# Kernel tuning notes

Measured on AMD Instinct MI355X. Metric: run time of the kernel, lower is better.

The kernel has to match this reference:

```python
import jax, jax.numpy as jnp
import numpy as np

B = 8
M = 500_000
XSIZE = 128


def setup_inputs() -> dict:
    key = jax.random.key(0)
    k1, k2 = jax.random.split(key)
    indices = jax.random.randint(k1, (B, M, 3), 0, XSIZE, dtype=jnp.int32)
    values = jax.random.normal(k2, (B, M), dtype=jnp.float32)
    return {"indices": indices, "values": values, "xsize": XSIZE}


def reference(indices, values, xsize):
    # Batched scatter-add density accumulation (tensor_scatter_nd_add per sample)
    def scatter_one(idx, val):
        grid = jnp.zeros((xsize, xsize, xsize), dtype=val.dtype)
        return grid.at[idx[:, 0], idx[:, 1], idx[:, 2]].add(val)

    grid = jax.vmap(scatter_one)(indices, values)  # (B, X, X, X)

    # Adjacent voxel differences along each spatial axis
    d1 = grid[:, 1:, :, :] - grid[:, :-1, :, :]
    d2 = grid[:, :, 1:, :] - grid[:, :, :-1, :]
    d3 = grid[:, :, :, 1:] - grid[:, :, :, :-1]

    ax = (1, 2, 3)
    # Total variation loss: normalized by total voxel count xsize^3
    num_pixels = jnp.float32(xsize * xsize * xsize)
    tv = (jnp.sum(jnp.abs(d1), axis=ax)
          + jnp.sum(jnp.abs(d2), axis=ax)
          + jnp.sum(jnp.abs(d3), axis=ax)) / num_pixels

    # MSE smoothness loss: normalizer matches TF code (2*X*X - X - X)
    num_pairs = jnp.float32(2 * xsize * xsize - 2 * xsize)
    mse = (jnp.sum(jnp.square(d1), axis=ax)
           + jnp.sum(jnp.square(d2), axis=ax)
           + jnp.sum(jnp.square(d3), axis=ax)) / num_pairs

    return jnp.stack([tv, mse])  # (2, B)
```

## Files before the change

### kernel.cpp

```cpp
#include <hip/hip_runtime.h>
#include <stdint.h>

#define BATCH 8
#define MPTS 500000
#define NPTS (BATCH * MPTS)
#define NBQ 1024
#define TP 16384
#define NTILE ((NPTS + TP - 1) / TP)
#define HROW (NBQ + 1)
#define NIFACE 304
#define NBND (BATCH * NIFACE)

template <int NT>
__device__ __forceinline__ void block_reduce2(float& tv, float& mse) {
    for (int off = 32; off > 0; off >>= 1) {
        tv  += __shfl_down(tv, off, 64);
        mse += __shfl_down(mse, off, 64);
    }
    __shared__ float stv[NT / 64], sms[NT / 64];
    int w = threadIdx.x >> 6, lane = threadIdx.x & 63;
    if (lane == 0) { stv[w] = tv; sms[w] = mse; }
    __syncthreads();
    if (threadIdx.x == 0) {
        float a = 0.f, m = 0.f;
        #pragma unroll
        for (int e = 0; e < NT / 64; ++e) { a += stv[e]; m += sms[e]; }
        tv = a; mse = m;
    }
}

__device__ __forceinline__ uint32_t pack_aux(int b, int i, int j, int k) {
    uint32_t q = ((uint32_t)b << 7) | ((uint32_t)(i >> 5) << 5) |
                 ((uint32_t)(j >> 5) << 3) | (uint32_t)(k >> 4);
    uint32_t l = ((uint32_t)(i & 31) << 9) | ((uint32_t)(j & 31) << 4) | (uint32_t)(k & 15);
    return (q << 14) | l;
}

__device__ __forceinline__ int gaddr(int s, int kl) {
    return s * 16 + (kl & 3) + ((((kl >> 2) ^ (s >> 1)) & 3) << 2);
}
__device__ __forceinline__ int goff(int s, int c) {
    return ((c ^ (s >> 1)) & 3) << 2;
}

__device__ __forceinline__ uint32_t val16(float f) {
    return (__float_as_uint(f) + 0x8000u) >> 16;
}

__global__ void __launch_bounds__(1024, 8) sort_k(const int* __restrict__ idx,
                                                  const float* __restrict__ val,
                                                  uint32_t* __restrict__ hoff,
                                                  uint32_t* __restrict__ rec) {
    __shared__ uint32_t h[NBQ];
    __shared__ uint32_t wtot[16];
    __shared__ uint32_t srt[TP];
    int tile = blockIdx.x;
    int p0 = tile * TP;
    int cnt = min(TP, NPTS - p0);
    h[threadIdx.x] = 0;
    __syncthreads();
    uint32_t a[16]; uint32_t vpk[8];
    int ng = cnt >> 2;
    #pragma unroll
    for (int e = 0; e < 4; ++e) {
        int g = threadIdx.x + e * 1024;
        if (g < ng) {
            int p = p0 + g * 4;
            const int4* ip = (const int4*)(idx + (size_t)p * 3);
            int4 A = ip[0], B = ip[1], C = ip[2];
            float4 V = *(const float4*)(val + p);
            int b = p / MPTS;
            a[4*e+0] = pack_aux(b, A.x, A.y, A.z);
            a[4*e+1] = pack_aux(b, A.w, B.x, B.y);
            a[4*e+2] = pack_aux(b, B.z, B.w, C.x);
            a[4*e+3] = pack_aux(b, C.y, C.z, C.w);
            vpk[2*e]     = val16(V.x) | (val16(V.y) << 16);
            vpk[2*e + 1] = val16(V.z) | (val16(V.w) << 16);
            #pragma unroll
            for (int u = 0; u < 4; ++u) atomicAdd(&h[a[4*e+u] >> 14], 1u);
        } else {
            a[4*e+0] = a[4*e+1] = a[4*e+2] = a[4*e+3] = 0xFFFFFFFFu;
            vpk[2*e] = vpk[2*e + 1] = 0u;
        }
    }
    __syncthreads();
    int q = threadIdx.x, lane = q & 63, wave = q >> 6;
    uint32_t cq = h[q];
    uint32_t inc = cq;
    #pragma unroll
    for (int off = 1; off < 64; off <<= 1) {
        uint32_t n = __shfl_up(inc, off, 64);
        if (lane >= off) inc += n;
    }
    if (lane == 63) wtot[wave] = inc;
    __syncthreads();
    if (q < 16) {
        uint32_t w = wtot[q];
        #pragma unroll
        for (int off = 1; off < 16; off <<= 1) {
            uint32_t n = __shfl_up(w, off, 16);
            if (q >= off) w += n;
        }
        wtot[q] = w;
    }
    __syncthreads();
    uint32_t lstart = (wave ? wtot[wave - 1] : 0u) + inc - cq;
    hoff[(size_t)tile * HROW + q] = lstart;
    if (q == 0) hoff[(size_t)tile * HROW + NBQ] = (uint32_t)cnt;
    h[q] = lstart;
    __syncthreads();
    #pragma unroll
    for (int e = 0; e < 16; ++e) {
        if (a[e] != 0xFFFFFFFFu) {
            uint32_t qq = a[e] >> 14;
            uint32_t u = (vpk[e >> 1] >> ((e & 1) * 16)) & 0xFFFFu;
            srt[atomicAdd(&h[qq], 1u)] = (u << 16) | (a[e] & 16383u);
        }
    }
    __syncthreads();
    uint4* recq = (uint4*)(rec + (size_t)tile * TP);
    const uint4* sr4 = (const uint4*)srt;
    for (int s = threadIdx.x; s < (cnt >> 2); s += 1024) recq[s] = sr4[s];
}

__global__ void __launch_bounds__(1024, 8) accum_k(const uint32_t* __restrict__ rec,
                                                   const uint32_t* __restrict__ hoff,
                                                   uint16_t* __restrict__ faces,
                                                   float2* __restrict__ pa) {
    __shared__ float g[16384];
    int qb = blockIdx.x;
    {
        float4 z = make_float4(0.f, 0.f, 0.f, 0.f);
        #pragma unroll
        for (int c = 0; c < 4; ++c)
            *(float4*)&g[(threadIdx.x + c * 1024) * 4] = z;
    }
    __syncthreads();
    {
        int grp = threadIdx.x >> 3;
        int r8  = threadIdx.x & 7;
        const uint32_t* rowA = hoff + (size_t)grp * HROW;
        uint32_t a0 = rowA[qb], a1 = rowA[qb + 1];
        const uint32_t* rpA = rec + (size_t)grp * TP;
        int tB = grp + 128;
        uint32_t b0 = 0, b1 = 0;
        const uint32_t* rpB = nullptr;
        if (tB < NTILE) {
            const uint32_t* rowB = hoff + (size_t)tB * HROW;
            b0 = rowB[qb]; b1 = rowB[qb + 1];
            rpB = rec + (size_t)tB * TP;
        }
        for (uint32_t r = a0 + r8; r < a1; r += 8) {
            uint32_t e = rpA[r];
            int l = e & 16383;
            atomicAdd(&g[gaddr(l >> 4, l & 15)], __uint_as_float(e & 0xFFFF0000u));
        }
        if (rpB) {
            for (uint32_t r = b0 + r8; r < b1; r += 8) {
                uint32_t e = rpB[r];
                int l = e & 16383;
                atomicAdd(&g[gaddr(l >> 4, l & 15)], __uint_as_float(e & 0xFFFF0000u));
            }
        }
    }
    __syncthreads();
    float tv = 0.f, mse = 0.f;
    {
        int s = threadIdx.x;
        int jl = s & 31, il = s >> 5;
        bool jin = jl < 31, iin = il < 31;
        float own[16];
        #pragma unroll
        for (int c = 0; c < 4; ++c)
            *(float4*)&own[c * 4] = *(const float4*)&g[s * 16 + goff(s, c)];
        #pragma unroll
        for (int k = 0; k < 15; ++k) {
            float d = own[k + 1] - own[k]; tv += fabsf(d); mse += d * d;
        }
        #pragma unroll
        for (int hh = 0; hh < 2; ++hh) {
            if (jin) {
                float jn[8];
                *(float4*)&jn[0] = *(const float4*)&g[(s + 1) * 16 + goff(s + 1, 2 * hh)];
                *(float4*)&jn[4] = *(const float4*)&g[(s + 1) * 16 + goff(s + 1, 2 * hh + 1)];
                #pragma unroll
                for (int k = 0; k < 8; ++k) {
                    float d = jn[k] - own[8 * hh + k]; tv += fabsf(d); mse += d * d;
                }
            }
            if (iin) {
                float inb[8];
                *(float4*)&inb[0] = *(const float4*)&g[(s + 32) * 16 + goff(s + 32, 2 * hh)];
                *(float4*)&inb[4] = *(const float4*)&g[(s + 32) * 16 + goff(s + 32, 2 * hh + 1)];
                #pragma unroll
                for (int k = 0; k < 8; ++k) {
                    float d = inb[k] - own[8 * hh + k]; tv += fabsf(d); mse += d * d;
                }
            }
        }
    }
    {
        uint16_t* f = faces + (size_t)qb * 4096;
        int t = threadIdx.x;
        if (t < 512) {
            int hi = t >> 4, lo = t & 15;
            f[t]        = (uint16_t)(__float_as_uint(g[gaddr(hi, lo)]) >> 16);
            f[512 + t]  = (uint16_t)(__float_as_uint(g[gaddr(992 + hi, lo)]) >> 16);
            f[1024 + t] = (uint16_t)(__float_as_uint(g[gaddr(hi * 32, lo)]) >> 16);
            f[1536 + t] = (uint16_t)(__float_as_uint(g[gaddr(hi * 32 + 31, lo)]) >> 16);
        }
        f[2048 + t] = (uint16_t)(__float_as_uint(g[gaddr(t, 0)]) >> 16);
        f[3072 + t] = (uint16_t)(__float_as_uint(g[gaddr(t, 15)]) >> 16);
    }
    block_reduce2<1024>(tv, mse);
    if (threadIdx.x == 0) pa[qb] = make_float2(tv, mse);
}

__device__ __forceinline__ float f16up(uint16_t u) {
    return __uint_as_float(((uint32_t)u) << 16);
}

__global__ void __launch_bounds__(256) boundary_k(const uint16_t* __restrict__ faces,
                                                  float2* __restrict__ pb) {
    int x = blockIdx.x;
    int b = x / NIFACE;
    int r = x - b * NIFACE;
    int qA, qB, fA, fB, elems;
    if (r < 96) {
        int s = r >> 5, u = (r >> 3) & 3, w = r & 7;
        qA = (b << 7) | (s << 5) | (u << 3) | w; qB = qA + 32;
        fA = 512; fB = 0; elems = 512;
    } else if (r < 192) {
        int r2 = r - 96;
        int s = r2 >> 5, u = (r2 >> 3) & 3, w = r2 & 7;
        qA = (b << 7) | (u << 5) | (s << 3) | w; qB = qA + 8;
        fA = 1536; fB = 1024; elems = 512;
    } else {
        int r2 = r - 192;
        int s = r2 >> 4, u = (r2 >> 2) & 3, v = r2 & 3;
        qA = (b << 7) | (u << 5) | (v << 3) | s; qB = qA + 1;
        fA = 3072; fB = 2048; elems = 1024;
    }
    const uint16_t* pA = faces + (size_t)qA * 4096 + fA;
    const uint16_t* pB = faces + (size_t)qB * 4096 + fB;
    float tv = 0.f, mse = 0.f;
    for (int e = threadIdx.x; e < elems; e += 256) {
        float d = f16up(pB[e]) - f16up(pA[e]);
        tv += fabsf(d); mse += d * d;
    }
    block_reduce2<256>(tv, mse);
    if (threadIdx.x == 0) pb[x] = make_float2(tv, mse);
}

__global__ void __launch_bounds__(256) final_k(const float2* __restrict__ pa,
                                               const float2* __restrict__ pb,
                                               float* __restrict__ out) {
    int b = blockIdx.x;
    float tv = 0.f, mse = 0.f;
    const float2* a = pa + (size_t)b * (NBQ / BATCH);
    for (int i = threadIdx.x; i < NBQ / BATCH; i += 256) { float2 v = a[i]; tv += v.x; mse += v.y; }
    const float2* p = pb + (size_t)b * NIFACE;
    for (int i = threadIdx.x; i < NIFACE; i += 256) { float2 v = p[i]; tv += v.x; mse += v.y; }
    block_reduce2<256>(tv, mse);
    if (threadIdx.x == 0) {
        out[b]     = tv  * (1.f / 2097152.f);
        out[8 + b] = mse * (1.f / 32512.f);
    }
}

extern "C" void kernel_launch(void* const* d_in, const int* in_sizes, int n_in,
                              void* d_out, int out_size, void* d_ws, size_t ws_size,
                              hipStream_t stream) {
    const int*   indices = (const int*)d_in[0];
    const float* values  = (const float*)d_in[1];
    float*       out     = (float*)d_out;

    char* wp = (char*)d_ws;
    uint32_t* hoff  = (uint32_t*)wp;
    wp += (((size_t)NTILE * HROW * 4) + 255) & ~(size_t)255;
    float2*   pa    = (float2*)wp;
    wp += (NBQ * 8 + 255) & ~(size_t)255;
    float2*   pb    = (float2*)wp;
    wp += ((size_t)NBND * 8 + 255) & ~(size_t)255;
    uint32_t* rec   = (uint32_t*)wp;
    wp += (((size_t)NTILE * TP * 4) + 255) & ~(size_t)255;
    uint16_t* faces = (uint16_t*)wp;

    sort_k    <<<NTILE, 1024, 0, stream>>>(indices, values, hoff, rec);
    accum_k   <<<NBQ,   1024, 0, stream>>>(rec, hoff, faces, pa);
    boundary_k<<<NBND,  256,  0, stream>>>(faces, pb);
    final_k   <<<BATCH, 256,  0, stream>>>(pa, pb, out);
}
```

Baseline: 136.1 us.

## Fuse all four stages into one cooperative persistent kernel with grid syncs

```diff
diff --git a/kernel.cpp b/kernel.cpp
--- a/kernel.cpp
+++ b/kernel.cpp
@@ -1,30 +1,34 @@
 #include <hip/hip_runtime.h>
+#include <hip/hip_cooperative_groups.h>
 #include <stdint.h>
 
 #define BATCH 8
 #define MPTS 500000
 #define NPTS (BATCH * MPTS)
 #define NBQ 1024
-#define TP 16384
+#define TP 8192
 #define NTILE ((NPTS + TP - 1) / TP)
 #define HROW (NBQ + 1)
 #define NIFACE 304
 #define NBND (BATCH * NIFACE)
-
-template <int NT>
+#define NT 512
+
+namespace cg = cooperative_groups;
+
+template <int NTT>
 __device__ __forceinline__ void block_reduce2(float& tv, float& mse) {
     for (int off = 32; off > 0; off >>= 1) {
         tv  += __shfl_down(tv, off, 64);
         mse += __shfl_down(mse, off, 64);
     }
-    __shared__ float stv[NT / 64], sms[NT / 64];
+    __shared__ float stv[NTT / 64], sms[NTT / 64];
     int w = threadIdx.x >> 6, lane = threadIdx.x & 63;
     if (lane == 0) { stv[w] = tv; sms[w] = mse; }
     __syncthreads();
     if (threadIdx.x == 0) {
         float a = 0.f, m = 0.f;
         #pragma unroll
-        for (int e = 0; e < NT / 64; ++e) { a += stv[e]; m += sms[e]; }
+        for (int e = 0; e < NTT / 64; ++e) { a += stv[e]; m += sms[e]; }
         tv = a; mse = m;
     }
 }
@@ -46,225 +50,222 @@
 __device__ __forceinline__ uint32_t val16(float f) {
     return (__float_as_uint(f) + 0x8000u) >> 16;
 }
-
-__global__ void __launch_bounds__(1024, 8) sort_k(const int* __restrict__ idx,
-                                                  const float* __restrict__ val,
-                                                  uint32_t* __restrict__ hoff,
-                                                  uint32_t* __restrict__ rec) {
-    __shared__ uint32_t h[NBQ];
-    __shared__ uint32_t wtot[16];
-    __shared__ uint32_t srt[TP];
-    int tile = blockIdx.x;
-    int p0 = tile * TP;
-    int cnt = min(TP, NPTS - p0);
-    h[threadIdx.x] = 0;
-    __syncthreads();
-    uint32_t a[16]; uint32_t vpk[8];
-    int ng = cnt >> 2;
-    #pragma unroll
-    for (int e = 0; e < 4; ++e) {
-        int g = threadIdx.x + e * 1024;
-        if (g < ng) {
-            int p = p0 + g * 4;
-            const int4* ip = (const int4*)(idx + (size_t)p * 3);
-            int4 A = ip[0], B = ip[1], C = ip[2];
-            float4 V = *(const float4*)(val + p);
-            int b = p / MPTS;
-            a[4*e+0] = pack_aux(b, A.x, A.y, A.z);
-            a[4*e+1] = pack_aux(b, A.w, B.x, B.y);
-            a[4*e+2] = pack_aux(b, B.z, B.w, C.x);
-            a[4*e+3] = pack_aux(b, C.y, C.z, C.w);
-            vpk[2*e]     = val16(V.x) | (val16(V.y) << 16);
-            vpk[2*e + 1] = val16(V.z) | (val16(V.w) << 16);
-            #pragma unroll
-            for (int u = 0; u < 4; ++u) atomicAdd(&h[a[4*e+u] >> 14], 1u);
-        } else {
-            a[4*e+0] = a[4*e+1] = a[4*e+2] = a[4*e+3] = 0xFFFFFFFFu;
-            vpk[2*e] = vpk[2*e + 1] = 0u;
-        }
-    }
-    __syncthreads();
-    int q = threadIdx.x, lane = q & 63, wave = q >> 6;
-    uint32_t cq = h[q];
-    uint32_t inc = cq;
-    #pragma unroll
-    for (int off = 1; off < 64; off <<= 1) {
-        uint32_t n = __shfl_up(inc, off, 64);
-        if (lane >= off) inc += n;
-    }
-    if (lane == 63) wtot[wave] = inc;
-    __syncthreads();
-    if (q < 16) {
-        uint32_t w = wtot[q];
-        #pragma unroll
-        for (int off = 1; off < 16; off <<= 1) {
-            uint32_t n = __shfl_up(w, off, 16);
-            if (q >= off) w += n;
-        }
-        wtot[q] = w;
-    }
-    __syncthreads();
-    uint32_t lstart = (wave ? wtot[wave - 1] : 0u) + inc - cq;
-    hoff[(size_t)tile * HROW + q] = lstart;
-    if (q == 0) hoff[(size_t)tile * HROW + NBQ] = (uint32_t)cnt;
-    h[q] = lstart;
-    __syncthreads();
-    #pragma unroll
-    for (int e = 0; e < 16; ++e) {
-        if (a[e] != 0xFFFFFFFFu) {
-            uint32_t qq = a[e] >> 14;
-            uint32_t u = (vpk[e >> 1] >> ((e & 1) * 16)) & 0xFFFFu;
-            srt[atomicAdd(&h[qq], 1u)] = (u << 16) | (a[e] & 16383u);
-        }
-    }
-    __syncthreads();
-    uint4* recq = (uint4*)(rec + (size_t)tile * TP);
-    const uint4* sr4 = (const uint4*)srt;
-    for (int s = threadIdx.x; s < (cnt >> 2); s += 1024) recq[s] = sr4[s];
-}
-
-__global__ void __launch_bounds__(1024, 8) accum_k(const uint32_t* __restrict__ rec,
-                                                   const uint32_t* __restrict__ hoff,
-                                                   uint16_t* __restrict__ faces,
-                                                   float2* __restrict__ pa) {
-    __shared__ float g[16384];
-    int qb = blockIdx.x;
-    {
-        float4 z = make_float4(0.f, 0.f, 0.f, 0.f);
-        #pragma unroll
-        for (int c = 0; c < 4; ++c)
-            *(float4*)&g[(threadIdx.x + c * 1024) * 4] = z;
-    }
-    __syncthreads();
-    {
-        int grp = threadIdx.x >> 3;
-        int r8  = threadIdx.x & 7;
-        const uint32_t* rowA = hoff + (size_t)grp * HROW;
-        uint32_t a0 = rowA[qb], a1 = rowA[qb + 1];
-        const uint32_t* rpA = rec + (size_t)grp * TP;
-        int tB = grp + 128;
-        uint32_t b0 = 0, b1 = 0;
-        const uint32_t* rpB = nullptr;
-        if (tB < NTILE) {
-            const uint32_t* rowB = hoff + (size_t)tB * HROW;
-            b0 = rowB[qb]; b1 = rowB[qb + 1];
-            rpB = rec + (size_t)tB * TP;
-        }
-        for (uint32_t r = a0 + r8; r < a1; r += 8) {
-            uint32_t e = rpA[r];
-            int l = e & 16383;
-            atomicAdd(&g[gaddr(l >> 4, l & 15)], __uint_as_float(e & 0xFFFF0000u));
-        }
-        if (rpB) {
-            for (uint32_t r = b0 + r8; r < b1; r += 8) {
-                uint32_t e = rpB[r];
-                int l = e & 16383;
-                atomicAdd(&g[gaddr(l >> 4, l & 15)], __uint_as_float(e & 0xFFFF0000u));
-            }
-        }
-    }
-    __syncthreads();
-    float tv = 0.f, mse = 0.f;
-    {
-        int s = threadIdx.x;
-        int jl = s & 31, il = s >> 5;
-        bool jin = jl < 31, iin = il < 31;
-        float own[16];
-        #pragma unroll
-        for (int c = 0; c < 4; ++c)
-            *(float4*)&own[c * 4] = *(const float4*)&g[s * 16 + goff(s, c)];
-        #pragma unroll
-        for (int k = 0; k < 15; ++k) {
-            float d = own[k + 1] - own[k]; tv += fabsf(d); mse += d * d;
-        }
-        #pragma unroll
-        for (int hh = 0; hh < 2; ++hh) {
-            if (jin) {
-                float jn[8];
-                *(float4*)&jn[0] = *(const float4*)&g[(s + 1) * 16 + goff(s + 1, 2 * hh)];
-                *(float4*)&jn[4] = *(const float4*)&g[(s + 1) * 16 + goff(s + 1, 2 * hh + 1)];
-                #pragma unroll
-                for (int k = 0; k < 8; ++k) {
-                    float d = jn[k] - own[8 * hh + k]; tv += fabsf(d); mse += d * d;
-                }
-            }
-            if (iin) {
-                float inb[8];
-                *(float4*)&inb[0] = *(const float4*)&g[(s + 32) * 16 + goff(s + 32, 2 * hh)];
-                *(float4*)&inb[4] = *(const float4*)&g[(s + 32) * 16 + goff(s + 32, 2 * hh + 1)];
-                #pragma unroll
-                for (int k = 0; k < 8; ++k) {
-                    float d = inb[k] - own[8 * hh + k]; tv += fabsf(d); mse += d * d;
-                }
-            }
-        }
-    }
-    {
-        uint16_t* f = faces + (size_t)qb * 4096;
-        int t = threadIdx.x;
-        if (t < 512) {
-            int hi = t >> 4, lo = t & 15;
-            f[t]        = (uint16_t)(__float_as_uint(g[gaddr(hi, lo)]) >> 16);
-            f[512 + t]  = (uint16_t)(__float_as_uint(g[gaddr(992 + hi, lo)]) >> 16);
-            f[1024 + t] = (uint16_t)(__float_as_uint(g[gaddr(hi * 32, lo)]) >> 16);
-            f[1536 + t] = (uint16_t)(__float_as_uint(g[gaddr(hi * 32 + 31, lo)]) >> 16);
-        }
-        f[2048 + t] = (uint16_t)(__float_as_uint(g[gaddr(t, 0)]) >> 16);
-        f[3072 + t] = (uint16_t)(__float_as_uint(g[gaddr(t, 15)]) >> 16);
-    }
-    block_reduce2<1024>(tv, mse);
-    if (threadIdx.x == 0) pa[qb] = make_float2(tv, mse);
-}
-
+__device__ __forceinline__ uint16_t top16(float f) {
+    return (uint16_t)(__float_as_uint(f) >> 16);
+}
 __device__ __forceinline__ float f16up(uint16_t u) {
     return __uint_as_float(((uint32_t)u) << 16);
 }
 
-__global__ void __launch_bounds__(256) boundary_k(const uint16_t* __restrict__ faces,
-                                                  float2* __restrict__ pb) {
-    int x = blockIdx.x;
-    int b = x / NIFACE;
-    int r = x - b * NIFACE;
-    int qA, qB, fA, fB, elems;
-    if (r < 96) {
-        int s = r >> 5, u = (r >> 3) & 3, w = r & 7;
-        qA = (b << 7) | (s << 5) | (u << 3) | w; qB = qA + 32;
-        fA = 512; fB = 0; elems = 512;
-    } else if (r < 192) {
-        int r2 = r - 96;
-        int s = r2 >> 5, u = (r2 >> 3) & 3, w = r2 & 7;
-        qA = (b << 7) | (u << 5) | (s << 3) | w; qB = qA + 8;
-        fA = 1536; fB = 1024; elems = 512;
-    } else {
-        int r2 = r - 192;
-        int s = r2 >> 4, u = (r2 >> 2) & 3, v = r2 & 3;
-        qA = (b << 7) | (u << 5) | (v << 3) | s; qB = qA + 1;
-        fA = 3072; fB = 2048; elems = 1024;
-    }
-    const uint16_t* pA = faces + (size_t)qA * 4096 + fA;
-    const uint16_t* pB = faces + (size_t)qB * 4096 + fB;
-    float tv = 0.f, mse = 0.f;
-    for (int e = threadIdx.x; e < elems; e += 256) {
-        float d = f16up(pB[e]) - f16up(pA[e]);
-        tv += fabsf(d); mse += d * d;
-    }
-    block_reduce2<256>(tv, mse);
-    if (threadIdx.x == 0) pb[x] = make_float2(tv, mse);
-}
-
-__global__ void __launch_bounds__(256) final_k(const float2* __restrict__ pa,
-                                               const float2* __restrict__ pb,
-                                               float* __restrict__ out) {
-    int b = blockIdx.x;
-    float tv = 0.f, mse = 0.f;
-    const float2* a = pa + (size_t)b * (NBQ / BATCH);
-    for (int i = threadIdx.x; i < NBQ / BATCH; i += 256) { float2 v = a[i]; tv += v.x; mse += v.y; }
-    const float2* p = pb + (size_t)b * NIFACE;
-    for (int i = threadIdx.x; i < NIFACE; i += 256) { float2 v = p[i]; tv += v.x; mse += v.y; }
-    block_reduce2<256>(tv, mse);
-    if (threadIdx.x == 0) {
-        out[b]     = tv  * (1.f / 2097152.f);
-        out[8 + b] = mse * (1.f / 32512.f);
+__global__ void __launch_bounds__(NT, 4) fused_k(const int* __restrict__ idx,
+                                                 const float* __restrict__ val,
+                                                 uint32_t* __restrict__ hoff,
+                                                 uint32_t* __restrict__ rec,
+                                                 uint16_t* __restrict__ faces,
+                                                 float2* __restrict__ pa,
+                                                 float2* __restrict__ pb,
+                                                 float* __restrict__ out) {
+    __shared__ float g[16384];
+    __shared__ uint32_t wtot[8];
+    uint32_t* h   = (uint32_t*)g;
+    uint32_t* srt = (uint32_t*)g + 1024;
+    cg::grid_group grid = cg::this_grid();
+    int tid = threadIdx.x;
+
+    for (int tile = blockIdx.x; tile < NTILE; tile += gridDim.x) {
+        int p0 = tile * TP;
+        int cnt = min(TP, NPTS - p0);
+        for (int c = tid; c < NBQ; c += NT) h[c] = 0;
+        __syncthreads();
+        uint32_t a[16]; uint32_t vpk[8];
+        int ng = cnt >> 2;
+        #pragma unroll
+        for (int e = 0; e < 4; ++e) {
+            int gg = tid + e * NT;
+            if (gg < ng) {
+                int p = p0 + gg * 4;
+                const int4* ip = (const int4*)(idx + (size_t)p * 3);
+                int4 A = ip[0], B = ip[1], C = ip[2];
+                float4 V = *(const float4*)(val + p);
+                int b = p / MPTS;
+                a[4*e+0] = pack_aux(b, A.x, A.y, A.z);
+                a[4*e+1] = pack_aux(b, A.w, B.x, B.y);
+                a[4*e+2] = pack_aux(b, B.z, B.w, C.x);
+                a[4*e+3] = pack_aux(b, C.y, C.z, C.w);
+                vpk[2*e]   = val16(V.x) | (val16(V.y) << 16);
+                vpk[2*e+1] = val16(V.z) | (val16(V.w) << 16);
+                #pragma unroll
+                for (int u = 0; u < 4; ++u) atomicAdd(&h[a[4*e+u] >> 14], 1u);
+            } else {
+                a[4*e+0] = a[4*e+1] = a[4*e+2] = a[4*e+3] = 0xFFFFFFFFu;
+                vpk[2*e] = vpk[2*e+1] = 0u;
+            }
+        }
+        __syncthreads();
+        int lane = tid & 63, wave = tid >> 6;
+        int q0 = tid * 2;
+        uint32_t c0 = h[q0], c1 = h[q0 + 1];
+        uint32_t ps = c0 + c1, inc = ps;
+        #pragma unroll
+        for (int off = 1; off < 64; off <<= 1) {
+            uint32_t n = __shfl_up(inc, off, 64);
+            if (lane >= off) inc += n;
+        }
+        if (lane == 63) wtot[wave] = inc;
+        __syncthreads();
+        if (tid < 8) {
+            uint32_t w = wtot[tid];
+            #pragma unroll
+            for (int off = 1; off < 8; off <<= 1) {
+                uint32_t n = __shfl_up(w, off, 8);
+                if (tid >= off) w += n;
+            }
+            wtot[tid] = w;
+        }
+        __syncthreads();
+        uint32_t pstart = (wave ? wtot[wave - 1] : 0u) + inc - ps;
+        uint32_t* hr = hoff + (size_t)tile * HROW;
+        hr[q0] = pstart; hr[q0 + 1] = pstart + c0;
+        if (tid == 0) hr[NBQ] = (uint32_t)cnt;
+        h[q0] = pstart; h[q0 + 1] = pstart + c0;
+        __syncthreads();
+        #pragma unroll
+        for (int e = 0; e < 16; ++e) {
+            if (a[e] != 0xFFFFFFFFu) {
+                uint32_t qq = a[e] >> 14;
+                uint32_t u = (vpk[e >> 1] >> ((e & 1) * 16)) & 0xFFFFu;
+                srt[atomicAdd(&h[qq], 1u)] = (u << 16) | (a[e] & 16383u);
+            }
+        }
+        __syncthreads();
+        uint4* recq = (uint4*)(rec + (size_t)tile * TP);
+        const uint4* sr4 = (const uint4*)srt;
+        for (int s = tid; s < (cnt >> 2); s += NT) recq[s] = sr4[s];
+        __syncthreads();
+    }
+    grid.sync();
+
+    for (int qb = blockIdx.x; qb < NBQ; qb += gridDim.x) {
+        {
+            float4 z = make_float4(0.f, 0.f, 0.f, 0.f);
+            #pragma unroll
+            for (int c = 0; c < 8; ++c)
+                *(float4*)&g[(tid + c * NT) * 4] = z;
+        }
+        __syncthreads();
+        {
+            int grp = tid >> 3, r8 = tid & 7;
+            for (int t = grp; t < NTILE; t += NT / 8) {
+                const uint32_t* row = hoff + (size_t)t * HROW;
+                uint32_t s0 = row[qb], s1 = row[qb + 1];
+                const uint32_t* rp = rec + (size_t)t * TP;
+                for (uint32_t r = s0 + r8; r < s1; r += 8) {
+                    uint32_t e = rp[r];
+                    int l = e & 16383;
+                    atomicAdd(&g[gaddr(l >> 4, l & 15)], __uint_as_float(e & 0xFFFF0000u));
+                }
+            }
+        }
+        __syncthreads();
+        float tv = 0.f, mse = 0.f;
+        #pragma unroll
+        for (int half = 0; half < 2; ++half) {
+            int s = tid + half * NT;
+            int jl = s & 31, il = s >> 5;
+            bool jin = jl < 31, iin = il < 31;
+            float own[16];
+            #pragma unroll
+            for (int c = 0; c < 4; ++c)
+                *(float4*)&own[c * 4] = *(const float4*)&g[s * 16 + goff(s, c)];
+            #pragma unroll
+            for (int k = 0; k < 15; ++k) {
+                float d = own[k + 1] - own[k]; tv += fabsf(d); mse += d * d;
+            }
+            #pragma unroll
+            for (int hh = 0; hh < 2; ++hh) {
+                if (jin) {
+                    float jn[8];
+                    *(float4*)&jn[0] = *(const float4*)&g[(s + 1) * 16 + goff(s + 1, 2 * hh)];
+                    *(float4*)&jn[4] = *(const float4*)&g[(s + 1) * 16 + goff(s + 1, 2 * hh + 1)];
+                    #pragma unroll
+                    for (int k = 0; k < 8; ++k) {
+                        float d = jn[k] - own[8 * hh + k]; tv += fabsf(d); mse += d * d;
+                    }
+                }
+                if (iin) {
+                    float inb[8];
+                    *(float4*)&inb[0] = *(const float4*)&g[(s + 32) * 16 + goff(s + 32, 2 * hh)];
+                    *(float4*)&inb[4] = *(const float4*)&g[(s + 32) * 16 + goff(s + 32, 2 * hh + 1)];
+                    #pragma unroll
+                    for (int k = 0; k < 8; ++k) {
+                        float d = inb[k] - own[8 * hh + k]; tv += fabsf(d); mse += d * d;
+                    }
+                }
+            }
+        }
+        {
+            uint16_t* f = faces + (size_t)qb * 4096;
+            int t = tid;
+            int hi = t >> 4, lo = t & 15;
+            f[t]        = top16(g[gaddr(hi, lo)]);
+            f[512 + t]  = top16(g[gaddr(992 + hi, lo)]);
+            f[1024 + t] = top16(g[gaddr(hi * 32, lo)]);
+            f[1536 + t] = top16(g[gaddr(hi * 32 + 31, lo)]);
+            f[2048 + t]      = top16(g[gaddr(t, 0)]);
+            f[2048 + NT + t] = top16(g[gaddr(t + NT, 0)]);
+            f[3072 + t]      = top16(g[gaddr(t, 15)]);
+            f[3072 + NT + t] = top16(g[gaddr(t + NT, 15)]);
+        }
+        block_reduce2<NT>(tv, mse);
+        if (tid == 0) pa[qb] = make_float2(tv, mse);
+        __syncthreads();
+    }
+    grid.sync();
+
+    for (int x = blockIdx.x; x < NBND; x += gridDim.x) {
+        int b = x / NIFACE;
+        int r = x - b * NIFACE;
+        int qA, qB, fA, fB, elems;
+        if (r < 96) {
+            int s = r >> 5, u = (r >> 3) & 3, w = r & 7;
+            qA = (b << 7) | (s << 5) | (u << 3) | w; qB = qA + 32;
+            fA = 512; fB = 0; elems = 512;
+        } else if (r < 192) {
+            int r2 = r - 96;
+            int s = r2 >> 5, u = (r2 >> 3) & 3, w = r2 & 7;
+            qA = (b << 7) | (u << 5) | (s << 3) | w; qB = qA + 8;
+            fA = 1536; fB = 1024; elems = 512;
+        } else {
+            int r2 = r - 192;
+            int s = r2 >> 4, u = (r2 >> 2) & 3, v = r2 & 3;
+            qA = (b << 7) | (u << 5) | (v << 3) | s; qB = qA + 1;
+            fA = 3072; fB = 2048; elems = 1024;
+        }
+        const uint16_t* pA = faces + (size_t)qA * 4096 + fA;
+        const uint16_t* pB = faces + (size_t)qB * 4096 + fB;
+        float tv = 0.f, mse = 0.f;
+        for (int e = tid; e < elems; e += NT) {
+            float d = f16up(pB[e]) - f16up(pA[e]);
+            tv += fabsf(d); mse += d * d;
+        }
+        block_reduce2<NT>(tv, mse);
+        if (tid == 0) pb[x] = make_float2(tv, mse);
+        __syncthreads();
+    }
+    grid.sync();
+
+    for (int b = blockIdx.x; b < BATCH; b += gridDim.x) {
+        float tv = 0.f, mse = 0.f;
+        const float2* A = pa + (size_t)b * (NBQ / BATCH);
+        for (int i = tid; i < NBQ / BATCH; i += NT) { float2 v2 = A[i]; tv += v2.x; mse += v2.y; }
+        const float2* P = pb + (size_t)b * NIFACE;
+        for (int i = tid; i < NIFACE; i += NT) { float2 v2 = P[i]; tv += v2.x; mse += v2.y; }
+        block_reduce2<NT>(tv, mse);
+        if (tid == 0) {
+            out[b]     = tv  * (1.f / 2097152.f);
+            out[8 + b] = mse * (1.f / 32512.f);
+        }
+        __syncthreads();
     }
 }
 
@@ -286,8 +287,13 @@
     wp += (((size_t)NTILE * TP * 4) + 255) & ~(size_t)255;
     uint16_t* faces = (uint16_t*)wp;
 
-    sort_k    <<<NTILE, 1024, 0, stream>>>(indices, values, hoff, rec);
-    accum_k   <<<NBQ,   1024, 0, stream>>>(rec, hoff, faces, pa);
-    boundary_k<<<NBND,  256,  0, stream>>>(faces, pb);
-    final_k   <<<BATCH, 256,  0, stream>>>(pa, pb, out);
-}
+    int maxPerCU = 0;
+    hipOccupancyMaxActiveBlocksPerMultiprocessor(&maxPerCU, fused_k, NT, 0);
+    if (maxPerCU < 1) maxPerCU = 1;
+    int nblk = maxPerCU * 256;
+    if (nblk > 512) nblk = 512;
+
+    void* args[] = { (void*)&indices, (void*)&values, (void*)&hoff, (void*)&rec,
+                     (void*)&faces, (void*)&pa, (void*)&pb, (void*)&out };
+    hipLaunchCooperativeKernel(fused_k, dim3(nblk), dim3(NT), args, 0u, stream);
+}
```

Result: slower. 256.4 us (+88.4%).
